# Kernel optimization log

Hardware: AMD Instinct MI355X
Metric: run time of the kernel (lower is better)

## Reference

```python
import jax, jax.numpy as jnp
import numpy as np
from jax import lax

EPS = 1e-5
K = 32
S1, S2 = 512, 256


def bn_relu(x, gamma, beta, axes):
    # BatchNorm in training mode (batch statistics, biased variance) + ReLU.
    mean = jnp.mean(x, axis=axes, keepdims=True)
    var = jnp.var(x, axis=axes, keepdims=True)
    return jax.nn.relu((x - mean) * lax.rsqrt(var + EPS) * gamma + beta)


def fps(xyz, s):
    # Farthest point sampling, deterministic start at index 0. xyz: [N,3] -> [s] indices
    N = xyz.shape[0]
    def body(carry, _):
        dist, far = carry
        d = jnp.sum((xyz - xyz[far]) ** 2, axis=-1)
        dist = jnp.minimum(dist, d)
        return (dist, jnp.argmax(dist).astype(jnp.int32)), far
    init = (jnp.full((N,), 1e10, xyz.dtype), jnp.int32(0))
    _, idx = lax.scan(body, init, None, length=s)
    return idx


def sample_and_knn_group(s, k, coords, features):
    # coords: [B,N,3], features: [B,N,D]
    fps_idx = jax.vmap(lambda c: fps(c, s))(coords)                      # [B,s]
    new_xyz = jnp.take_along_axis(coords, fps_idx[..., None], axis=1)   # [B,s,3]
    new_feat = jnp.take_along_axis(features, fps_idx[..., None], axis=1)  # [B,s,D]
    # squared euclidean distances [B,s,N]
    d2 = (jnp.sum(new_xyz ** 2, -1)[..., None]
          - 2.0 * jnp.einsum('bsc,bnc->bsn', new_xyz, coords)
          + jnp.sum(coords ** 2, -1)[:, None, :])
    _, knn_idx = lax.top_k(-d2, k)                                       # [B,s,k]
    grouped = jax.vmap(lambda f, i: f[i])(features, knn_idx)             # [B,s,k,D]
    rel = grouped - new_feat[:, :, None, :]
    agg = jnp.concatenate([rel, jnp.broadcast_to(new_feat[:, :, None, :], rel.shape)], axis=-1)  # [B,s,k,2D]
    return new_xyz, agg


def sg_block(s, coords, feats, w1, cb1, g1, b1, w2, cb2, g2, b2):
    new_xyz, agg = sample_and_knn_group(s, K, coords, feats)
    h = bn_relu(jnp.einsum('bskc,oc->bsko', agg, w1) + cb1, g1, b1, (0, 1, 2))
    h = bn_relu(jnp.einsum('bskc,oc->bsko', h, w2) + cb2, g2, b2, (0, 1, 2))
    return new_xyz, jnp.max(h, axis=2)  # max over k neighbors -> [B,s,O]


def setup_inputs() -> dict:
    key = jax.random.key(0)
    ks = jax.random.split(key, 8)
    B, N = 16, 2048
    sc = 0.05
    return {
        'x': jax.random.normal(ks[0], (B, 3, N), jnp.float32),
        'emb_w1': jax.random.normal(ks[1], (64, 3), jnp.float32) * sc,
        'emb_g1': jnp.ones((64,), jnp.float32), 'emb_b1': jnp.zeros((64,), jnp.float32),
        'emb_w2': jax.random.normal(ks[2], (64, 64), jnp.float32) * sc,
        'emb_g2': jnp.ones((64,), jnp.float32), 'emb_b2': jnp.zeros((64,), jnp.float32),
        'sg1_w1': jax.random.normal(ks[3], (128, 128), jnp.float32) * sc,
        'sg1_cb1': jnp.zeros((128,), jnp.float32),
        'sg1_g1': jnp.ones((128,), jnp.float32), 'sg1_b1': jnp.zeros((128,), jnp.float32),
        'sg1_w2': jax.random.normal(ks[4], (128, 128), jnp.float32) * sc,
        'sg1_cb2': jnp.zeros((128,), jnp.float32),
        'sg1_g2': jnp.ones((128,), jnp.float32), 'sg1_b2': jnp.zeros((128,), jnp.float32),
        'sg2_w1': jax.random.normal(ks[5], (512, 256), jnp.float32) * sc,
        'sg2_cb1': jnp.zeros((512,), jnp.float32),
        'sg2_g1': jnp.ones((512,), jnp.float32), 'sg2_b1': jnp.zeros((512,), jnp.float32),
        'sg2_w2': jax.random.normal(ks[6], (512, 512), jnp.float32) * sc,
        'sg2_cb2': jnp.zeros((512,), jnp.float32),
        'sg2_g2': jnp.ones((512,), jnp.float32), 'sg2_b2': jnp.zeros((512,), jnp.float32),
    }


def reference(x, emb_w1, emb_g1, emb_b1, emb_w2, emb_g2, emb_b2,
              sg1_w1, sg1_cb1, sg1_g1, sg1_b1, sg1_w2, sg1_cb2, sg1_g2, sg1_b2,
              sg2_w1, sg2_cb1, sg2_g1, sg2_b1, sg2_w2, sg2_cb2, sg2_g2, sg2_b2):
    xyz = jnp.transpose(x, (0, 2, 1))  # [B,N,3]
    f = bn_relu(jnp.einsum('bnc,oc->bno', xyz, emb_w1), emb_g1, emb_b1, (0, 1))   # [B,N,64]
    f = bn_relu(jnp.einsum('bnc,oc->bno', f, emb_w2), emb_g2, emb_b2, (0, 1))
    xyz1, f1 = sg_block(S1, xyz, f, sg1_w1, sg1_cb1, sg1_g1, sg1_b1,
                        sg1_w2, sg1_cb2, sg1_g2, sg1_b2)   # [B,512,128]
    _, f2 = sg_block(S2, xyz1, f1, sg2_w1, sg2_cb1, sg2_g1, sg2_b1,
                     sg2_w2, sg2_cb2, sg2_g2, sg2_b2)      # [B,256,512]
    return jnp.transpose(f2, (0, 2, 1))  # [B,512,256] to match torch [B,C,s]
```

## Files before the change

kernel.cpp:

```cpp
#include <hip/hip_runtime.h>
#include <hip/hip_bf16.h>

#define EPS_BN 1e-5f
constexpr int BB = 16, NN = 2048, SS1 = 512, SS2 = 256, KNb = 32;

typedef short bf16x8 __attribute__((ext_vector_type(8)));
typedef float f32x4 __attribute__((ext_vector_type(4)));

__device__ inline float bflo(unsigned u) { return __uint_as_float(u << 16); }
__device__ inline float bfhi(unsigned u) { return __uint_as_float(u & 0xffff0000u); }
__device__ inline unsigned short f2bf_bits(float v) {
  __hip_bfloat16 h = __float2bfloat16(v);
  return *reinterpret_cast<unsigned short*>(&h);
}
__device__ inline unsigned fmono(float v) {
  int b = __float_as_int(v);
  return (unsigned)(b ^ ((b >> 31) | 0x80000000));
}
__device__ inline unsigned bn2(unsigned u, float s0, float h0, float s1, float h1) {
  float v0 = fmaxf(bflo(u) * s0 + h0, 0.f);
  float v1 = fmaxf(bfhi(u) * s1 + h1, 0.f);
  return (unsigned)f2bf_bits(v0) | ((unsigned)f2bf_bits(v1) << 16);
}

template <int CTRL>
__device__ inline void dpp_step_min(unsigned& hi, unsigned& lo) {
  unsigned hs = (unsigned)__builtin_amdgcn_update_dpp((int)hi, (int)hi, CTRL, 0xF, 0xF, false);
  unsigned ls = (unsigned)__builtin_amdgcn_update_dpp((int)lo, (int)lo, CTRL, 0xF, 0xF, false);
  bool take = (hs < hi) || (hs == hi && ls < lo);
  hi = take ? hs : hi; lo = take ? ls : lo;
}
template <int CTRL>
__device__ inline void dpp_step_maxv_minidx(unsigned& hi, unsigned& lo) {
  unsigned hs = (unsigned)__builtin_amdgcn_update_dpp((int)hi, (int)hi, CTRL, 0xF, 0xF, false);
  unsigned ls = (unsigned)__builtin_amdgcn_update_dpp((int)lo, (int)lo, CTRL, 0xF, 0xF, false);
  bool take = (hs > hi) || (hs == hi && ls < lo);
  hi = take ? hs : hi; lo = take ? ls : lo;
}
__device__ inline void dpp_chain_min(unsigned& hi, unsigned& lo) {
  dpp_step_min<0x111>(hi, lo); dpp_step_min<0x112>(hi, lo);
  dpp_step_min<0x114>(hi, lo); dpp_step_min<0x118>(hi, lo);
  dpp_step_min<0x142>(hi, lo); dpp_step_min<0x143>(hi, lo);
}
__device__ inline void dpp_chain_maxv_minidx(unsigned& hi, unsigned& lo) {
  dpp_step_maxv_minidx<0x111>(hi, lo); dpp_step_maxv_minidx<0x112>(hi, lo);
  dpp_step_maxv_minidx<0x114>(hi, lo); dpp_step_maxv_minidx<0x118>(hi, lo);
  dpp_step_maxv_minidx<0x142>(hi, lo); dpp_step_maxv_minidx<0x143>(hi, lo);
}
__device__ inline int dpp_reduce_min_idx(unsigned hi, unsigned lo) {
  dpp_chain_min(hi, lo);
  return __builtin_amdgcn_readlane((int)lo, 63);
}

__global__ __launch_bounds__(256, 1) void k_mega1(
    const float* __restrict__ x, const float* __restrict__ emb_w1,
    float* __restrict__ fA, double* __restrict__ rsE1, double* __restrict__ rqE1,
    int* __restrict__ fps1, float* __restrict__ nx1,
    int* __restrict__ fps2, float* __restrict__ nx2,
    const float* __restrict__ w11f, __hip_bfloat16* __restrict__ wb11,
    const float* __restrict__ w12f, __hip_bfloat16* __restrict__ wb12,
    const float* __restrict__ w21f, __hip_bfloat16* __restrict__ wb21,
    const float* __restrict__ w22f, __hip_bfloat16* __restrict__ wb22) {
  int blk = blockIdx.x;
  int t = threadIdx.x;
  if (blk < BB) {
    constexpr int PPL = NN / 256;
    constexpr int PPL2 = SS1 / 256;
    int b = blk; int w = t >> 6;
    __shared__ float4 sxyz[NN];
    __shared__ float4 c4[SS1];
    __shared__ unsigned combH[2][4], combL[2][4];
    float px[PPL], py[PPL], pz[PPL], ds[PPL];
#pragma unroll
    for (int r = 0; r < PPL; r++) {
      int i = r * 256 + t;
      float xx = x[(size_t)(b * 3 + 0) * NN + i];
      float yy = x[(size_t)(b * 3 + 1) * NN + i];
      float zz = x[(size_t)(b * 3 + 2) * NN + i];
      px[r] = xx; py[r] = yy; pz[r] = zz;
      float ox = xx, oy = yy, oz = zz;
      asm volatile("" : "+v"(ox), "+v"(oy), "+v"(oz));
      float4 o4 = {ox, oy, oz, 0.f};
      sxyz[i] = o4;
      ds[r] = 1e10f;
    }
    __syncthreads();
    int far = 0; int p = 0;
    for (int it = 0; it < SS1; it++) {
      float4 f4 = sxyz[far];
      float fx = f4.x, fy = f4.y, fz = f4.z;
      if (t == 0) {
        fps1[b * SS1 + it] = far;
        size_t ob = ((size_t)b * SS1 + it) * 3;
        nx1[ob] = fx; nx1[ob + 1] = fy; nx1[ob + 2] = fz;
        c4[it] = f4;
      }
      float mm0 = -1.f, mm1 = -1.f, mm2 = -1.f, mm3 = -1.f;
#pragma unroll
      for (int r = 0; r < PPL; r++) {
        float dx = px[r] - fx, dy = py[r] - fy, dz = pz[r] - fz;
        float d = dx * dx + dy * dy + dz * dz;
        float nd = d < ds[r] ? d : ds[r];
        ds[r] = nd;
        if ((r & 3) == 0) mm0 = nd > mm0 ? nd : mm0;
        else if ((r & 3) == 1) mm1 = nd > mm1 ? nd : mm1;
        else if ((r & 3) == 2) mm2 = nd > mm2 ? nd : mm2;
        else mm3 = nd > mm3 ? nd : mm3;
      }
      float m = fmaxf(fmaxf(mm0, mm1), fmaxf(mm2, mm3));
      int cand[PPL];
#pragma unroll
      for (int r = 0; r < PPL; r++) cand[r] = (ds[r] == m) ? (r * 256 + t) : 0x7fffffff;
#pragma unroll
      for (int st = PPL / 2; st > 0; st >>= 1)
#pragma unroll
        for (int r = 0; r < st; r++) cand[r] = cand[r] < cand[r + st] ? cand[r] : cand[r + st];
      unsigned hi = __float_as_uint(m);
      unsigned lo = (unsigned)cand[0];
      dpp_chain_maxv_minidx(hi, lo);
      unsigned rh = (unsigned)__builtin_amdgcn_readlane((int)hi, 63);
      unsigned rl = (unsigned)__builtin_amdgcn_readlane((int)lo, 63);
      combH[p][w] = rh; combL[p][w] = rl;
      __syncthreads();
      unsigned bh = combH[p][0], bl = combL[p][0];
#pragma unroll
      for (int ww = 1; ww < 4; ww++) {
        unsigned oh = combH[p][ww], ol = combL[p][ww];
        bool take = (oh > bh) || (oh == bh && ol < bl);
        bh = take ? oh : bh; bl = take ? ol : bl;
      }
      far = (int)bl;
      p ^= 1;
    }
    __syncthreads();
    float qx[PPL2], qy[PPL2], qz[PPL2], es[PPL2];
#pragma unroll
    for (int r = 0; r < PPL2; r++) {
      float4 v = c4[r * 256 + t];
      qx[r] = v.x; qy[r] = v.y; qz[r] = v.z; es[r] = 1e10f;
    }
    int far2 = 0;
    for (int it = 0; it < SS2; it++) {
      float4 f4 = c4[far2];
      float fx = f4.x, fy = f4.y, fz = f4.z;
      if (t == 0) {
        fps2[b * SS2 + it] = far2;
        size_t ob = ((size_t)b * SS2 + it) * 3;
        nx2[ob] = fx; nx2[ob + 1] = fy; nx2[ob + 2] = fz;
      }
      float mm0, mm1;
      { float dx = qx[0] - fx, dy = qy[0] - fy, dz = qz[0] - fz;
        float d = dx * dx + dy * dy + dz * dz;
        float nd = d < es[0] ? d : es[0]; es[0] = nd; mm0 = nd; }
      { float dx = qx[1] - fx, dy = qy[1] - fy, dz = qz[1] - fz;
        float d = dx * dx + dy * dy + dz * dz;
        float nd = d < es[1] ? d : es[1]; es[1] = nd; mm1 = nd; }
      float m = fmaxf(mm0, mm1);
      int c0 = (es[0] == m) ? t : 0x7fffffff;
      int c1 = (es[1] == m) ? (256 + t) : 0x7fffffff;
      int cnd = c0 < c1 ? c0 : c1;
      unsigned hi = __float_as_uint(m), lo = (unsigned)cnd;
      dpp_chain_maxv_minidx(hi, lo);
      unsigned rh = (unsigned)__builtin_amdgcn_readlane((int)hi, 63);
      unsigned rl = (unsigned)__builtin_amdgcn_readlane((int)lo, 63);
      combH[p][w] = rh; combL[p][w] = rl;
      __syncthreads();
      unsigned bh = combH[p][0], bl = combL[p][0];
#pragma unroll
      for (int ww = 1; ww < 4; ww++) {
        unsigned oh = combH[p][ww], ol = combL[p][ww];
        bool take = (oh > bh) || (oh == bh && ol < bl);
        bh = take ? oh : bh; bl = take ? ol : bl;
      }
      far2 = (int)bl;
      p ^= 1;
    }
    return;
  }
  blk -= BB;
  if (blk < 8192) {
    __shared__ float ls[64], lq[64];
    if (t < 64) { ls[t] = 0.f; lq[t] = 0.f; }
    __syncthreads();
    int o = t & 63;
    int pt = blk * 4 + (t >> 6);
    int b = pt >> 11, n = pt & (NN - 1);
    float x0 = x[(size_t)(b * 3 + 0) * NN + n];
    float x1 = x[(size_t)(b * 3 + 1) * NN + n];
    float x2 = x[(size_t)(b * 3 + 2) * NN + n];
    float v = x0 * emb_w1[o * 3] + x1 * emb_w1[o * 3 + 1] + x2 * emb_w1[o * 3 + 2];
    fA[(size_t)pt * 64 + o] = v;
    atomicAdd(&ls[o], v);
    atomicAdd(&lq[o], v * v);
    __syncthreads();
    if (t < 64) {
      int rep = blk & 63;
      atomicAdd(&rsE1[(size_t)rep * 64 + t], (double)ls[t]);
      atomicAdd(&rqE1[(size_t)rep * 64 + t], (double)lq[t]);
    }
    return;
  }
  blk -= 8192;
  if (blk < 64) { int i = blk * 256 + t; wb11[i] = __float2bfloat16(w11f[i]); return; }
  blk -= 64;
  if (blk < 64) { int i = blk * 256 + t; wb12[i] = __float2bfloat16(w12f[i]); return; }
  blk -= 64;
  if (blk < 512) { int i = blk * 256 + t; wb21[i] = __float2bfloat16(w21f[i]); return; }
  blk -= 512;
  { int i = blk * 256 + t; wb22[i] = __float2bfloat16(w22f[i]); }
}

__global__ __launch_bounds__(256) void k_mega2(
    const float* __restrict__ x, const float* __restrict__ nx1, int* __restrict__ knn1,
    const float* __restrict__ fA, const float* __restrict__ sce1,
    const float* __restrict__ she1, const float* __restrict__ w2,
    float* __restrict__ fB, double* __restrict__ rsE2, double* __restrict__ rqE2) {
  int blk = blockIdx.x; int t = threadIdx.x;
  if (blk < 2048) {
    constexpr int PPL = NN / 64;
    int lane = t & 63;
    int center = blk * 4 + (t >> 6);
    int b = center >> 9;
    float cx = nx1[(size_t)center * 3], cy = nx1[(size_t)center * 3 + 1],
          cz = nx1[(size_t)center * 3 + 2];
    float cn = cx * cx + cy * cy + cz * cz;
    float d2[PPL];
#pragma unroll
    for (int r = 0; r < PPL; r++) {
      int i = r * 64 + lane;
      float xx = x[(size_t)(b * 3 + 0) * NN + i];
      float yy = x[(size_t)(b * 3 + 1) * NN + i];
      float zz = x[(size_t)(b * 3 + 2) * NN + i];
      d2[r] = cn - 2.f * (cx * xx + cy * yy + cz * zz) + (xx * xx + yy * yy + zz * zz);
    }
    for (int kk = 0; kk < KNb; kk++) {
      float a0 = d2[0], a1 = d2[1], a2 = d2[2], a3 = d2[3];
#pragma unroll
      for (int r = 4; r < PPL; r += 4) {
        a0 = fminf(a0, d2[r]); a1 = fminf(a1, d2[r + 1]);
        a2 = fminf(a2, d2[r + 2]); a3 = fminf(a3, d2[r + 3]);
      }
      float m = fminf(fminf(a0, a1), fminf(a2, a3));
      int cand[PPL];
#pragma unroll
      for (int r = 0; r < PPL; r++) cand[r] = (d2[r] == m) ? (r * 64 + lane) : 0x7fffffff;
#pragma unroll
      for (int st = PPL / 2; st > 0; st >>= 1)
#pragma unroll
        for (int r = 0; r < st; r++) cand[r] = cand[r] < cand[r + st] ? cand[r] : cand[r + st];
      int widx = dpp_reduce_min_idx(fmono(m), (unsigned)cand[0]);
      if (lane == 0) knn1[(size_t)center * KNb + kk] = widx;
      int wr = widx >> 6, wl = widx & 63;
#pragma unroll
      for (int r = 0; r < PPL; r++) d2[r] = (r == wr && lane == wl) ? 3.4e38f : d2[r];
    }
    return;
  }
  blk -= 2048;
  __shared__ float wT[64][65];
  __shared__ float fs[4][64];
  __shared__ float ss[64], sq[64];
#pragma unroll
  for (int k = 0; k < 16; k++) {
    int idx = k * 256 + t;
    wT[idx & 63][idx >> 6] = w2[idx];
  }
  if (t < 64) { ss[t] = 0.f; sq[t] = 0.f; }
  int pt0 = blk * 4;
  {
    float v = fA[(size_t)pt0 * 64 + t];
    int c = t & 63;
    v = fmaxf(v * sce1[c] + she1[c], 0.f);
    fs[t >> 6][c] = v;
  }
  __syncthreads();
  int o = t & 63, pq = t >> 6;
  float acc = 0.f;
#pragma unroll 8
  for (int c = 0; c < 64; c++) acc += fs[pq][c] * wT[c][o];
  fB[(size_t)pt0 * 64 + t] = acc;
  atomicAdd(&ss[o], acc);
  atomicAdd(&sq[o], acc * acc);
  __syncthreads();
  if (t < 64) {
    int rep = blk & 63;
    atomicAdd(&rsE2[(size_t)rep * 64 + t], (double)ss[t]);
    atomicAdd(&rqE2[(size_t)rep * 64 + t], (double)sq[t]);
  }
}

template <int N, int S>
__global__ __launch_bounds__(256) void k_knn4(const float* __restrict__ pts,
                                              const float* __restrict__ ctr,
                                              int* __restrict__ knn) {
  constexpr int PPL = N / 64;
  int lane = threadIdx.x & 63;
  int center = blockIdx.x * 4 + (threadIdx.x >> 6);
  int b = center / S;
  float cx = ctr[(size_t)center * 3], cy = ctr[(size_t)center * 3 + 1],
        cz = ctr[(size_t)center * 3 + 2];
  float cn = cx * cx + cy * cy + cz * cz;
  float d2[PPL];
#pragma unroll
  for (int r = 0; r < PPL; r++) {
    int i = r * 64 + lane;
    size_t pb = ((size_t)b * N + i) * 3;
    float xx = pts[pb], yy = pts[pb + 1], zz = pts[pb + 2];
    d2[r] = cn - 2.f * (cx * xx + cy * yy + cz * zz) + (xx * xx + yy * yy + zz * zz);
  }
  for (int kk = 0; kk < KNb; kk++) {
    float a0 = d2[0], a1 = d2[1], a2 = d2[2], a3 = d2[3];
#pragma unroll
    for (int r = 4; r < PPL; r += 4) {
      a0 = fminf(a0, d2[r]); a1 = fminf(a1, d2[r + 1]);
      a2 = fminf(a2, d2[r + 2]); a3 = fminf(a3, d2[r + 3]);
    }
    float m = fminf(fminf(a0, a1), fminf(a2, a3));
    int cand[PPL];
#pragma unroll
    for (int r = 0; r < PPL; r++) cand[r] = (d2[r] == m) ? (r * 64 + lane) : 0x7fffffff;
#pragma unroll
    for (int st = PPL / 2; st > 0; st >>= 1)
#pragma unroll
      for (int r = 0; r < st; r++) cand[r] = cand[r] < cand[r + st] ? cand[r] : cand[r + st];
    int widx = dpp_reduce_min_idx(fmono(m), (unsigned)cand[0]);
    if (lane == 0) knn[(size_t)center * KNb + kk] = widx;
    int wr = widx >> 6, wl = widx & 63;
#pragma unroll
    for (int r = 0; r < PPL; r++) d2[r] = (r == wr && lane == wl) ? 3.4e38f : d2[r];
  }
}

template <int D, bool BN>
__global__ __launch_bounds__(256) void k_gather(const float* __restrict__ feat, int N,
                                                const int* __restrict__ fpsidx,
                                                const int* __restrict__ knn, int S,
                                                const float* __restrict__ bnsc,
                                                const float* __restrict__ bnsh,
                                                __hip_bfloat16* __restrict__ A) {
  int blk = blockIdx.x; int b = blk / S; int t = threadIdx.x;
  __shared__ float cf[D]; __shared__ int nbr[KNb];
  if (t < KNb) nbr[t] = knn[(size_t)blk * KNb + t];
  int center = fpsidx[blk];
  for (int c = t; c < D; c += 256) {
    float v = feat[((size_t)b * N + center) * D + c];
    if constexpr (BN) v = fmaxf(v * bnsc[c] + bnsh[c], 0.f);
    cf[c] = v;
  }
  __syncthreads();
  for (int i = t; i < KNb * D; i += 256) {
    int kk = i / D, c = i - kk * D;
    float v = feat[((size_t)b * N + nbr[kk]) * D + c];
    if constexpr (BN) v = fmaxf(v * bnsc[c] + bnsh[c], 0.f);
    size_t row = (size_t)blk * KNb + kk;
    A[row * (2 * D) + c] = __float2bfloat16(v - cf[c]);
    A[row * (2 * D) + D + c] = __float2bfloat16(cf[c]);
  }
}

template <int K, int EPI, bool BNA>
__global__ __launch_bounds__(256) void k_mgemm(
    const __hip_bfloat16* __restrict__ A, const __hip_bfloat16* __restrict__ W,
    int N, int Mtiles, const float* __restrict__ bias,
    const float* __restrict__ bnsc, const float* __restrict__ bnsh,
    __hip_bfloat16* __restrict__ Hout,
    float* __restrict__ maxb, float* __restrict__ minb,
    double* __restrict__ rsum, double* __restrict__ rsq) {
  constexpr int SP = 40;
  int bm = blockIdx.x % Mtiles; int bn = blockIdx.x / Mtiles;
  int t = threadIdx.x; int w = t >> 6; int lane = t & 63;
  int wm = w & 1, wn = w >> 1; int quad = lane >> 4; int l15 = lane & 15;
  __shared__ short As[128 * SP];
  __shared__ short Ws[128 * SP];
  __shared__ float scs[BNA ? K : 1], shs[BNA ? K : 1];
  if constexpr (BNA) {
    for (int i = t; i < K; i += 256) { scs[i] = bnsc[i]; shs[i] = bnsh[i]; }
  }
  f32x4 acc[4][4];
  f32x4 zero = {0.f, 0.f, 0.f, 0.f};
#pragma unroll
  for (int i = 0; i < 4; i++)
#pragma unroll
    for (int j = 0; j < 4; j++) acc[i][j] = zero;

  int srow = t >> 2, sseg = t & 3;
  const short* Ag = (const short*)A;
  const short* Wg = (const short*)W;
  size_t arow0 = (size_t)bm * 128;
  size_t wrow0 = (size_t)bn * 128;

  for (int k0 = 0; k0 < K; k0 += 32) {
    __syncthreads();
    uint4 a0 = *(const uint4*)(Ag + (arow0 + srow) * K + k0 + sseg * 8);
    uint4 a1 = *(const uint4*)(Ag + (arow0 + srow + 64) * K + k0 + sseg * 8);
    uint4 b0 = *(const uint4*)(Wg + (wrow0 + srow) * K + k0 + sseg * 8);
    uint4 b1 = *(const uint4*)(Wg + (wrow0 + srow + 64) * K + k0 + sseg * 8);
    if constexpr (BNA) {
      int cb = k0 + sseg * 8;
      float s[8], h[8];
#pragma unroll
      for (int q = 0; q < 8; q++) { s[q] = scs[cb + q]; h[q] = shs[cb + q]; }
      a0.x = bn2(a0.x, s[0], h[0], s[1], h[1]);
      a0.y = bn2(a0.y, s[2], h[2], s[3], h[3]);
      a0.z = bn2(a0.z, s[4], h[4], s[5], h[5]);
      a0.w = bn2(a0.w, s[6], h[6], s[7], h[7]);
      a1.x = bn2(a1.x, s[0], h[0], s[1], h[1]);
      a1.y = bn2(a1.y, s[2], h[2], s[3], h[3]);
      a1.z = bn2(a1.z, s[4], h[4], s[5], h[5]);
      a1.w = bn2(a1.w, s[6], h[6], s[7], h[7]);
    }
    *(uint4*)(As + srow * SP + sseg * 8) = a0;
    *(uint4*)(As + (srow + 64) * SP + sseg * 8) = a1;
    *(uint4*)(Ws + srow * SP + sseg * 8) = b0;
    *(uint4*)(Ws + (srow + 64) * SP + sseg * 8) = b1;
    __syncthreads();
    bf16x8 af[4], bfr[4];
#pragma unroll
    for (int i = 0; i < 4; i++)
      af[i] = *(const bf16x8*)(As + (wm * 64 + i * 16 + l15) * SP + quad * 8);
#pragma unroll
    for (int j = 0; j < 4; j++)
      bfr[j] = *(const bf16x8*)(Ws + (wn * 64 + j * 16 + l15) * SP + quad * 8);
#pragma unroll
    for (int i = 0; i < 4; i++)
#pragma unroll
      for (int j = 0; j < 4; j++)
        acc[i][j] = __builtin_amdgcn_mfma_f32_16x16x32_bf16(af[i], bfr[j], acc[i][j], 0, 0, 0);
  }

  if constexpr (EPI == 0) {
    int rep = blockIdx.x & 63;
#pragma unroll
    for (int j = 0; j < 4; j++) {
      int col = bn * 128 + wn * 64 + j * 16 + l15;
      float bs = bias[col];
      float su = 0.f, sq = 0.f;
#pragma unroll
      for (int i = 0; i < 4; i++)
#pragma unroll
        for (int r = 0; r < 4; r++) {
          int row = bm * 128 + wm * 64 + i * 16 + quad * 4 + r;
          float v = acc[i][j][r] + bs;
          Hout[(size_t)row * N + col] = __float2bfloat16(v);
          su += v; sq += v * v;
        }
      atomicAdd(&rsum[(size_t)rep * N + col], (double)su);
      atomicAdd(&rsq[(size_t)rep * N + col], (double)sq);
    }
  } else {
    __shared__ float buf[128][33];
    for (int s = 0; s < 4; s++) {
      __syncthreads();
      if (wn == (s >> 1)) {
        int jb = 2 * (s & 1);
#pragma unroll
        for (int jj = 0; jj < 2; jj++) {
          int j = jb + jj;
          int lcol = jj * 16 + l15;
          float bs = bias[bn * 128 + s * 32 + lcol];
#pragma unroll
          for (int i = 0; i < 4; i++)
#pragma unroll
            for (int r = 0; r < 4; r++)
              buf[wm * 64 + i * 16 + quad * 4 + r][lcol] = acc[i][j][r] + bs;
        }
      }
      __syncthreads();
      if (t < 128) {
        int g = t >> 5, c = t & 31;
        float mx = -3.4e38f, mn = 3.4e38f, su = 0.f, sq = 0.f;
#pragma unroll
        for (int r = 0; r < 32; r++) {
          float v = buf[g * 32 + r][c];
          mx = fmaxf(mx, v); mn = fminf(mn, v);
          su += v; sq += v * v;
        }
        int col = bn * 128 + s * 32 + c;
        size_t gidx = (size_t)bm * 4 + g;
        maxb[gidx * N + col] = mx;
        minb[gidx * N + col] = mn;
        int rep = blockIdx.x & 63;
        atomicAdd(&rsum[(size_t)rep * N + col], (double)su);
        atomicAdd(&rsq[(size_t)rep * N + col], (double)sq);
      }
    }
  }
}

__global__ void k_finalize(const double* __restrict__ rsum, const double* __restrict__ rsq,
                           int O, int rows,
                           const float* __restrict__ gamma, const float* __restrict__ beta,
                           float* __restrict__ scale, float* __restrict__ shift) {
  int o = blockIdx.x * blockDim.x + threadIdx.x;
  if (o >= O) return;
  double s = 0, s2 = 0;
  for (int r = 0; r < 64; r++) { s += rsum[(size_t)r * O + o]; s2 += rsq[(size_t)r * O + o]; }
  double mean = s / rows;
  double var = s2 / rows - mean * mean;
  float sc = gamma[o] * rsqrtf((float)var + EPS_BN);
  scale[o] = sc; shift[o] = beta[o] - (float)mean * sc;
}

__global__ void k_final_feat(const float* __restrict__ maxb, const float* __restrict__ minb,
                             const float* __restrict__ scale, const float* __restrict__ shift,
                             float* __restrict__ out, int total, int O) {
  int idx = blockIdx.x * blockDim.x + threadIdx.x;
  if (idx >= total) return;
  int o = idx % O; float sc = scale[o];
  float sel = sc > 0.f ? maxb[idx] : minb[idx];
  out[idx] = fmaxf(sel * sc + shift[o], 0.f);
}

__global__ void k_final_out(const float* __restrict__ maxb, const float* __restrict__ minb,
                            const float* __restrict__ scale, const float* __restrict__ shift,
                            float* __restrict__ out) {
  int idx = blockIdx.x * blockDim.x + threadIdx.x;
  if (idx >= BB * SS2 * 512) return;
  int o = idx % 512; int si = (idx / 512) % SS2; int b = idx / (512 * SS2);
  float sc = scale[o];
  float sel = sc > 0.f ? maxb[idx] : minb[idx];
  out[((size_t)b * 512 + o) * SS2 + si] = fmaxf(sel * sc + shift[o], 0.f);
}

extern "C" void kernel_launch(void* const* d_in, const int* in_sizes, int n_in,
                              void* d_out, int out_size, void* d_ws, size_t ws_size,
                              hipStream_t stream) {
  const float* x       = (const float*)d_in[0];
  const float* emb_w1  = (const float*)d_in[1];
  const float* emb_g1  = (const float*)d_in[2];
  const float* emb_b1  = (const float*)d_in[3];
  const float* emb_w2  = (const float*)d_in[4];
  const float* emb_g2  = (const float*)d_in[5];
  const float* emb_b2  = (const float*)d_in[6];
  const float* sg1_w1  = (const float*)d_in[7];
  const float* sg1_cb1 = (const float*)d_in[8];
  const float* sg1_g1  = (const float*)d_in[9];
  const float* sg1_b1  = (const float*)d_in[10];
  const float* sg1_w2  = (const float*)d_in[11];
  const float* sg1_cb2 = (const float*)d_in[12];
  const float* sg1_g2  = (const float*)d_in[13];
  const float* sg1_b2  = (const float*)d_in[14];
  const float* sg2_w1  = (const float*)d_in[15];
  const float* sg2_cb1 = (const float*)d_in[16];
  const float* sg2_g1  = (const float*)d_in[17];
  const float* sg2_b1  = (const float*)d_in[18];
  const float* sg2_w2  = (const float*)d_in[19];
  const float* sg2_cb2 = (const float*)d_in[20];
  const float* sg2_g2  = (const float*)d_in[21];
  const float* sg2_b2  = (const float*)d_in[22];

  char* ws = (char*)d_ws;
  size_t off = 0;
  auto alloc = [&](size_t bytes) -> size_t {
    size_t cur = off; off += (bytes + 255) & ~(size_t)255; return cur;
  };
  float* fA   = (float*)(ws + alloc((size_t)BB * NN * 64 * 4));
  float* fB   = (float*)(ws + alloc((size_t)BB * NN * 64 * 4));
  float* f1   = (float*)(ws + alloc((size_t)BB * SS1 * 128 * 4));
  float* nx1  = (float*)(ws + alloc((size_t)BB * SS1 * 3 * 4));
  float* nx2  = (float*)(ws + alloc((size_t)BB * SS2 * 3 * 4));
  int* fps1   = (int*)(ws + alloc((size_t)BB * SS1 * 4));
  int* fps2   = (int*)(ws + alloc((size_t)BB * SS2 * 4));
  int* knn1   = (int*)(ws + alloc((size_t)BB * SS1 * KNb * 4));
  int* knn2   = (int*)(ws + alloc((size_t)BB * SS2 * KNb * 4));
  float* maxb = (float*)(ws + alloc((size_t)BB * SS2 * 512 * 4));
  float* minb = (float*)(ws + alloc((size_t)BB * SS2 * 512 * 4));
  float* scbuf = (float*)(ws + alloc((size_t)12 * 512 * 4));
  float* sc11 = scbuf + 4 * 512, *sh11 = scbuf + 5 * 512;
  float* sc12 = scbuf + 6 * 512, *sh12 = scbuf + 7 * 512;
  float* sc21 = scbuf + 8 * 512, *sh21 = scbuf + 9 * 512;
  float* sc22 = scbuf + 10 * 512, *sh22 = scbuf + 11 * 512;
  float* sc_e1 = scbuf + 0 * 512, *sh_e1 = scbuf + 1 * 512;
  float* sc_e2 = scbuf + 2 * 512, *sh_e2 = scbuf + 3 * 512;
  size_t statsz = (size_t)12 * 64 * 512 * 8;
  char* statz = ws + alloc(statsz);
  double* st = (double*)statz;
  double* rsA = st + 0 * 64 * 512, *rqA = st + 1 * 64 * 512;
  double* rsB = st + 2 * 64 * 512, *rqB = st + 3 * 64 * 512;
  double* rsC = st + 4 * 64 * 512, *rqC = st + 5 * 64 * 512;
  double* rsD = st + 6 * 64 * 512, *rqD = st + 7 * 64 * 512;
  double* rsE1 = st + 8 * 64 * 512, *rqE1 = st + 9 * 64 * 512;
  double* rsE2 = st + 10 * 64 * 512, *rqE2 = st + 11 * 64 * 512;
  __hip_bfloat16* wb11 = (__hip_bfloat16*)(ws + alloc(128 * 128 * 2));
  __hip_bfloat16* wb12 = (__hip_bfloat16*)(ws + alloc(128 * 128 * 2));
  __hip_bfloat16* wb21 = (__hip_bfloat16*)(ws + alloc(512 * 256 * 2));
  __hip_bfloat16* wb22 = (__hip_bfloat16*)(ws + alloc(512 * 512 * 2));
  __hip_bfloat16* Abuf = (__hip_bfloat16*)(ws + alloc((size_t)262144 * 128 * 2));
  __hip_bfloat16* Hbuf = (__hip_bfloat16*)(ws + alloc((size_t)131072 * 512 * 2));

  hipMemsetAsync(statz, 0, statsz, stream);

  const int thr = 256;
  k_mega1<<<9872, 256, 0, stream>>>(x, emb_w1, fA, rsE1, rqE1, fps1, nx1, fps2, nx2,
                                    sg1_w1, wb11, sg1_w2, wb12, sg2_w1, wb21, sg2_w2, wb22);
  k_finalize<<<1, 64, 0, stream>>>(rsE1, rqE1, 64, BB * NN, emb_g1, emb_b1, sc_e1, sh_e1);
  k_mega2<<<10240, 256, 0, stream>>>(x, nx1, knn1, fA, sc_e1, sh_e1, emb_w2,
                                     fB, rsE2, rqE2);
  k_finalize<<<1, 64, 0, stream>>>(rsE2, rqE2, 64, BB * NN, emb_g2, emb_b2, sc_e2, sh_e2);

  k_gather<64, true><<<BB * SS1, 256, 0, stream>>>(fB, NN, fps1, knn1, SS1,
                                                   sc_e2, sh_e2, Abuf);
  k_mgemm<128, 0, false><<<2048, 256, 0, stream>>>(Abuf, wb11, 128, 2048, sg1_cb1,
                                                   nullptr, nullptr, Hbuf,
                                                   nullptr, nullptr, rsA, rqA);
  k_finalize<<<1, 128, 0, stream>>>(rsA, rqA, 128, 262144, sg1_g1, sg1_b1, sc11, sh11);
  k_mgemm<128, 1, true><<<2048, 256, 0, stream>>>(Hbuf, wb12, 128, 2048, sg1_cb2,
                                                  sc11, sh11, nullptr,
                                                  maxb, minb, rsB, rqB);
  k_finalize<<<1, 128, 0, stream>>>(rsB, rqB, 128, 262144, sg1_g2, sg1_b2, sc12, sh12);
  k_final_feat<<<(BB * SS1 * 128 + thr - 1) / thr, thr, 0, stream>>>(maxb, minb, sc12, sh12,
                                                                     f1, BB * SS1 * 128, 128);

  k_knn4<SS1, SS2><<<BB * SS2 / 4, 256, 0, stream>>>(nx1, nx2, knn2);

  k_gather<128, false><<<BB * SS2, 256, 0, stream>>>(f1, SS1, fps2, knn2, SS2,
                                                     nullptr, nullptr, Abuf);
  k_mgemm<256, 0, false><<<1024 * 4, 256, 0, stream>>>(Abuf, wb21, 512, 1024, sg2_cb1,
                                                       nullptr, nullptr, Hbuf,
                                                       nullptr, nullptr, rsC, rqC);
  k_finalize<<<4, 128, 0, stream>>>(rsC, rqC, 512, 131072, sg2_g1, sg2_b1, sc21, sh21);
  k_mgemm<512, 1, true><<<1024 * 4, 256, 0, stream>>>(Hbuf, wb22, 512, 1024, sg2_cb2,
                                                      sc21, sh21, nullptr,
                                                      maxb, minb, rsD, rqD);
  k_finalize<<<4, 128, 0, stream>>>(rsD, rqD, 512, 131072, sg2_g2, sg2_b2, sc22, sh22);
  k_final_out<<<(BB * SS2 * 512 + thr - 1) / thr, thr, 0, stream>>>(maxb, minb, sc22, sh22,
                                                                    (float*)d_out);
}
```

Measured before the change: 1.253 ms.

## Fuse second-stage kNN into mega2, fold final_feat into gather, single-wave FPS2

The second FPS loop now runs on one wavefront with 8 points per lane, so the per-iteration block barrier and LDS combine step go away. The stage-2 kNN kernel is folded into k_mega2 as an extra block range. The emb conv2 part now handles 16 points per block, which shrinks the grid. k_final_feat and the generic gather are replaced by a gather that applies the BN+ReLU on the fly from maxb/minb, dropping the f1 intermediate and two launches. In exchange, the BN transform is recomputed per gathered neighbor and the emb blocks take on more serial work each.

```diff
diff --git a/kernel.cpp b/kernel.cpp
--- a/kernel.cpp
+++ b/kernel.cpp
@@ -65,7 +65,6 @@
   int t = threadIdx.x;
   if (blk < BB) {
     constexpr int PPL = NN / 256;
-    constexpr int PPL2 = SS1 / 256;
     int b = blk; int w = t >> 6;
     __shared__ float4 sxyz[NN];
     __shared__ float4 c4[SS1];
@@ -133,47 +132,46 @@
       p ^= 1;
     }
     __syncthreads();
-    float qx[PPL2], qy[PPL2], qz[PPL2], es[PPL2];
-#pragma unroll
-    for (int r = 0; r < PPL2; r++) {
-      float4 v = c4[r * 256 + t];
+    if (t >= 64) return;
+    int lane = t;
+    float qx[8], qy[8], qz[8], es[8];
+#pragma unroll
+    for (int r = 0; r < 8; r++) {
+      float4 v = c4[r * 64 + lane];
       qx[r] = v.x; qy[r] = v.y; qz[r] = v.z; es[r] = 1e10f;
     }
     int far2 = 0;
     for (int it = 0; it < SS2; it++) {
       float4 f4 = c4[far2];
       float fx = f4.x, fy = f4.y, fz = f4.z;
-      if (t == 0) {
+      if (lane == 0) {
         fps2[b * SS2 + it] = far2;
         size_t ob = ((size_t)b * SS2 + it) * 3;
         nx2[ob] = fx; nx2[ob + 1] = fy; nx2[ob + 2] = fz;
       }
-      float mm0, mm1;
-      { float dx = qx[0] - fx, dy = qy[0] - fy, dz = qz[0] - fz;
+      float mm0 = -1.f, mm1 = -1.f, mm2 = -1.f, mm3 = -1.f;
+#pragma unroll
+      for (int r = 0; r < 8; r++) {
+        float dx = qx[r] - fx, dy = qy[r] - fy, dz = qz[r] - fz;
         float d = dx * dx + dy * dy + dz * dz;
-        float nd = d < es[0] ? d : es[0]; es[0] = nd; mm0 = nd; }
-      { float dx = qx[1] - fx, dy = qy[1] - fy, dz = qz[1] - fz;
-        float d = dx * dx + dy * dy + dz * dz;
-        float nd = d < es[1] ? d : es[1]; es[1] = nd; mm1 = nd; }
-      float m = fmaxf(mm0, mm1);
-      int c0 = (es[0] == m) ? t : 0x7fffffff;
-      int c1 = (es[1] == m) ? (256 + t) : 0x7fffffff;
-      int cnd = c0 < c1 ? c0 : c1;
-      unsigned hi = __float_as_uint(m), lo = (unsigned)cnd;
+        float nd = d < es[r] ? d : es[r];
+        es[r] = nd;
+        if ((r & 3) == 0) mm0 = nd > mm0 ? nd : mm0;
+        else if ((r & 3) == 1) mm1 = nd > mm1 ? nd : mm1;
+        else if ((r & 3) == 2) mm2 = nd > mm2 ? nd : mm2;
+        else mm3 = nd > mm3 ? nd : mm3;
+      }
+      float m = fmaxf(fmaxf(mm0, mm1), fmaxf(mm2, mm3));
+      int cand[8];
+#pragma unroll
+      for (int r = 0; r < 8; r++) cand[r] = (es[r] == m) ? (r * 64 + lane) : 0x7fffffff;
+#pragma unroll
+      for (int st = 4; st > 0; st >>= 1)
+#pragma unroll
+        for (int r = 0; r < st; r++) cand[r] = cand[r] < cand[r + st] ? cand[r] : cand[r + st];
+      unsigned hi = __float_as_uint(m), lo = (unsigned)cand[0];
       dpp_chain_maxv_minidx(hi, lo);
-      unsigned rh = (unsigned)__builtin_amdgcn_readlane((int)hi, 63);
-      unsigned rl = (unsigned)__builtin_amdgcn_readlane((int)lo, 63);
-      combH[p][w] = rh; combL[p][w] = rl;
-      __syncthreads();
-      unsigned bh = combH[p][0], bl = combL[p][0];
-#pragma unroll
-      for (int ww = 1; ww < 4; ww++) {
-        unsigned oh = combH[p][ww], ol = combL[p][ww];
-        bool take = (oh > bh) || (oh == bh && ol < bl);
-        bh = take ? oh : bh; bl = take ? ol : bl;
-      }
-      far2 = (int)bl;
-      p ^= 1;
+      far2 = __builtin_amdgcn_readlane((int)lo, 63);
     }
     return;
   }
@@ -212,6 +210,7 @@
 
 __global__ __launch_bounds__(256) void k_mega2(
     const float* __restrict__ x, const float* __restrict__ nx1, int* __restrict__ knn1,
+    const float* __restrict__ nx2, int* __restrict__ knn2,
     const float* __restrict__ fA, const float* __restrict__ sce1,
     const float* __restrict__ she1, const float* __restrict__ w2,
     float* __restrict__ fB, double* __restrict__ rsE2, double* __restrict__ rqE2) {
@@ -257,8 +256,45 @@
     return;
   }
   blk -= 2048;
+  if (blk < 1024) {
+    constexpr int PPL = SS1 / 64;
+    int lane = t & 63;
+    int center = blk * 4 + (t >> 6);
+    int b = center >> 8;
+    float cx = nx2[(size_t)center * 3], cy = nx2[(size_t)center * 3 + 1],
+          cz = nx2[(size_t)center * 3 + 2];
+    float cn = cx * cx + cy * cy + cz * cz;
+    float d2[PPL];
+#pragma unroll
+    for (int r = 0; r < PPL; r++) {
+      int i = r * 64 + lane;
+      size_t pb = ((size_t)b * SS1 + i) * 3;
+      float xx = nx1[pb], yy = nx1[pb + 1], zz = nx1[pb + 2];
+      d2[r] = cn - 2.f * (cx * xx + cy * yy + cz * zz) + (xx * xx + yy * yy + zz * zz);
+    }
+    for (int kk = 0; kk < KNb; kk++) {
+      float a0 = d2[0], a1 = d2[1], a2 = d2[2], a3 = d2[3];
+      a0 = fminf(a0, d2[4]); a1 = fminf(a1, d2[5]);
+      a2 = fminf(a2, d2[6]); a3 = fminf(a3, d2[7]);
+      float m = fminf(fminf(a0, a1), fminf(a2, a3));
+      int cand[PPL];
+#pragma unroll
+      for (int r = 0; r < PPL; r++) cand[r] = (d2[r] == m) ? (r * 64 + lane) : 0x7fffffff;
+#pragma unroll
+      for (int st = PPL / 2; st > 0; st >>= 1)
+#pragma unroll
+        for (int r = 0; r < st; r++) cand[r] = cand[r] < cand[r + st] ? cand[r] : cand[r + st];
+      int widx = dpp_reduce_min_idx(fmono(m), (unsigned)cand[0]);
+      if (lane == 0) knn2[(size_t)center * KNb + kk] = widx;
+      int wr = widx >> 6, wl = widx & 63;
+#pragma unroll
+      for (int r = 0; r < PPL; r++) d2[r] = (r == wr && lane == wl) ? 3.4e38f : d2[r];
+    }
+    return;
+  }
+  blk -= 1024;
   __shared__ float wT[64][65];
-  __shared__ float fs[4][64];
+  __shared__ float fs[16][64];
   __shared__ float ss[64], sq[64];
 #pragma unroll
   for (int k = 0; k < 16; k++) {
@@ -266,68 +302,32 @@
     wT[idx & 63][idx >> 6] = w2[idx];
   }
   if (t < 64) { ss[t] = 0.f; sq[t] = 0.f; }
-  int pt0 = blk * 4;
-  {
-    float v = fA[(size_t)pt0 * 64 + t];
-    int c = t & 63;
+  int pt0 = blk * 16;
+#pragma unroll
+  for (int it = 0; it < 4; it++) {
+    int idx = it * 256 + t;
+    int p = idx >> 6, c = idx & 63;
+    float v = fA[(size_t)(pt0 + p) * 64 + c];
     v = fmaxf(v * sce1[c] + she1[c], 0.f);
-    fs[t >> 6][c] = v;
+    fs[p][c] = v;
   }
   __syncthreads();
-  int o = t & 63, pq = t >> 6;
-  float acc = 0.f;
+#pragma unroll
+  for (int it = 0; it < 4; it++) {
+    int idx = it * 256 + t;
+    int p = idx >> 6, o = idx & 63;
+    float acc = 0.f;
 #pragma unroll 8
-  for (int c = 0; c < 64; c++) acc += fs[pq][c] * wT[c][o];
-  fB[(size_t)pt0 * 64 + t] = acc;
-  atomicAdd(&ss[o], acc);
-  atomicAdd(&sq[o], acc * acc);
+    for (int c = 0; c < 64; c++) acc += fs[p][c] * wT[c][o];
+    fB[(size_t)(pt0 + p) * 64 + o] = acc;
+    atomicAdd(&ss[o], acc);
+    atomicAdd(&sq[o], acc * acc);
+  }
   __syncthreads();
   if (t < 64) {
     int rep = blk & 63;
     atomicAdd(&rsE2[(size_t)rep * 64 + t], (double)ss[t]);
     atomicAdd(&rqE2[(size_t)rep * 64 + t], (double)sq[t]);
-  }
-}
-
-template <int N, int S>
-__global__ __launch_bounds__(256) void k_knn4(const float* __restrict__ pts,
-                                              const float* __restrict__ ctr,
-                                              int* __restrict__ knn) {
-  constexpr int PPL = N / 64;
-  int lane = threadIdx.x & 63;
-  int center = blockIdx.x * 4 + (threadIdx.x >> 6);
-  int b = center / S;
-  float cx = ctr[(size_t)center * 3], cy = ctr[(size_t)center * 3 + 1],
-        cz = ctr[(size_t)center * 3 + 2];
-  float cn = cx * cx + cy * cy + cz * cz;
-  float d2[PPL];
-#pragma unroll
-  for (int r = 0; r < PPL; r++) {
-    int i = r * 64 + lane;
-    size_t pb = ((size_t)b * N + i) * 3;
-    float xx = pts[pb], yy = pts[pb + 1], zz = pts[pb + 2];
-    d2[r] = cn - 2.f * (cx * xx + cy * yy + cz * zz) + (xx * xx + yy * yy + zz * zz);
-  }
-  for (int kk = 0; kk < KNb; kk++) {
-    float a0 = d2[0], a1 = d2[1], a2 = d2[2], a3 = d2[3];
-#pragma unroll
-    for (int r = 4; r < PPL; r += 4) {
-      a0 = fminf(a0, d2[r]); a1 = fminf(a1, d2[r + 1]);
-      a2 = fminf(a2, d2[r + 2]); a3 = fminf(a3, d2[r + 3]);
-    }
-    float m = fminf(fminf(a0, a1), fminf(a2, a3));
-    int cand[PPL];
-#pragma unroll
-    for (int r = 0; r < PPL; r++) cand[r] = (d2[r] == m) ? (r * 64 + lane) : 0x7fffffff;
-#pragma unroll
-    for (int st = PPL / 2; st > 0; st >>= 1)
-#pragma unroll
-      for (int r = 0; r < st; r++) cand[r] = cand[r] < cand[r + st] ? cand[r] : cand[r + st];
-    int widx = dpp_reduce_min_idx(fmono(m), (unsigned)cand[0]);
-    if (lane == 0) knn[(size_t)center * KNb + kk] = widx;
-    int wr = widx >> 6, wl = widx & 63;
-#pragma unroll
-    for (int r = 0; r < PPL; r++) d2[r] = (r == wr && lane == wl) ? 3.4e38f : d2[r];
   }
 }
 
@@ -355,6 +355,35 @@
     size_t row = (size_t)blk * KNb + kk;
     A[row * (2 * D) + c] = __float2bfloat16(v - cf[c]);
     A[row * (2 * D) + D + c] = __float2bfloat16(cf[c]);
+  }
+}
+
+__global__ __launch_bounds__(256) void k_gather_feat(
+    const float* __restrict__ maxb, const float* __restrict__ minb,
+    const float* __restrict__ sc, const float* __restrict__ sh,
+    const int* __restrict__ fpsidx, const int* __restrict__ knn,
+    __hip_bfloat16* __restrict__ A) {
+  constexpr int D = 128;
+  int blk = blockIdx.x; int b = blk / SS2; int t = threadIdx.x;
+  __shared__ float cf[D]; __shared__ int nbr[KNb];
+  if (t < KNb) nbr[t] = knn[(size_t)blk * KNb + t];
+  int center = fpsidx[blk];
+  for (int c = t; c < D; c += 256) {
+    size_t row = (size_t)b * SS1 + center;
+    float s = sc[c];
+    float sel = s > 0.f ? maxb[row * D + c] : minb[row * D + c];
+    cf[c] = fmaxf(sel * s + sh[c], 0.f);
+  }
+  __syncthreads();
+  for (int i = t; i < KNb * D; i += 256) {
+    int kk = i / D, c = i - kk * D;
+    size_t row = (size_t)b * SS1 + nbr[kk];
+    float s = sc[c];
+    float sel = s > 0.f ? maxb[row * D + c] : minb[row * D + c];
+    float v = fmaxf(sel * s + sh[c], 0.f);
+    size_t orow = (size_t)blk * KNb + kk;
+    A[orow * (2 * D) + c] = __float2bfloat16(v - cf[c]);
+    A[orow * (2 * D) + D + c] = __float2bfloat16(cf[c]);
   }
 }
 
@@ -499,16 +528,6 @@
   double var = s2 / rows - mean * mean;
   float sc = gamma[o] * rsqrtf((float)var + EPS_BN);
   scale[o] = sc; shift[o] = beta[o] - (float)mean * sc;
-}
-
-__global__ void k_final_feat(const float* __restrict__ maxb, const float* __restrict__ minb,
-                             const float* __restrict__ scale, const float* __restrict__ shift,
-                             float* __restrict__ out, int total, int O) {
-  int idx = blockIdx.x * blockDim.x + threadIdx.x;
-  if (idx >= total) return;
-  int o = idx % O; float sc = scale[o];
-  float sel = sc > 0.f ? maxb[idx] : minb[idx];
-  out[idx] = fmaxf(sel * sc + shift[o], 0.f);
 }
 
 __global__ void k_final_out(const float* __restrict__ maxb, const float* __restrict__ minb,
@@ -556,7 +575,6 @@
   };
   float* fA   = (float*)(ws + alloc((size_t)BB * NN * 64 * 4));
   float* fB   = (float*)(ws + alloc((size_t)BB * NN * 64 * 4));
-  float* f1   = (float*)(ws + alloc((size_t)BB * SS1 * 128 * 4));
   float* nx1  = (float*)(ws + alloc((size_t)BB * SS1 * 3 * 4));
   float* nx2  = (float*)(ws + alloc((size_t)BB * SS2 * 3 * 4));
   int* fps1   = (int*)(ws + alloc((size_t)BB * SS1 * 4));
@@ -594,8 +612,8 @@
   k_mega1<<<9872, 256, 0, stream>>>(x, emb_w1, fA, rsE1, rqE1, fps1, nx1, fps2, nx2,
                                     sg1_w1, wb11, sg1_w2, wb12, sg2_w1, wb21, sg2_w2, wb22);
   k_finalize<<<1, 64, 0, stream>>>(rsE1, rqE1, 64, BB * NN, emb_g1, emb_b1, sc_e1, sh_e1);
-  k_mega2<<<10240, 256, 0, stream>>>(x, nx1, knn1, fA, sc_e1, sh_e1, emb_w2,
-                                     fB, rsE2, rqE2);
+  k_mega2<<<5120, 256, 0, stream>>>(x, nx1, knn1, nx2, knn2, fA, sc_e1, sh_e1, emb_w2,
+                                    fB, rsE2, rqE2);
   k_finalize<<<1, 64, 0, stream>>>(rsE2, rqE2, 64, BB * NN, emb_g2, emb_b2, sc_e2, sh_e2);
 
   k_gather<64, true><<<BB * SS1, 256, 0, stream>>>(fB, NN, fps1, knn1, SS1,
@@ -608,13 +626,8 @@
                                                   sc11, sh11, nullptr,
                                                   maxb, minb, rsB, rqB);
   k_finalize<<<1, 128, 0, stream>>>(rsB, rqB, 128, 262144, sg1_g2, sg1_b2, sc12, sh12);
-  k_final_feat<<<(BB * SS1 * 128 + thr - 1) / thr, thr, 0, stream>>>(maxb, minb, sc12, sh12,
-                                                                     f1, BB * SS1 * 128, 128);
-
-  k_knn4<SS1, SS2><<<BB * SS2 / 4, 256, 0, stream>>>(nx1, nx2, knn2);
-
-  k_gather<128, false><<<BB * SS2, 256, 0, stream>>>(f1, SS1, fps2, knn2, SS2,
-                                                     nullptr, nullptr, Abuf);
+
+  k_gather_feat<<<BB * SS2, 256, 0, stream>>>(maxb, minb, sc12, sh12, fps2, knn2, Abuf);
   k_mgemm<256, 0, false><<<1024 * 4, 256, 0, stream>>>(Abuf, wb21, 512, 1024, sg2_cb1,
                                                        nullptr, nullptr, Hbuf,
                                                        nullptr, nullptr, rsC, rqC);
```

Result: faster. 1.212 ms (-3.3%).
